# Kernel tuning notes

Measured on AMD Instinct MI355X. Metric: run time of the kernel, lower is better.

The kernel has to match this reference:

```python
import jax, jax.numpy as jnp
import numpy as np

B, N, HN, HE, H = 8, 128, 256, 128, 8
DH = HN // H
P = N * (N - 1) // 2


def _ln(x, g, b, eps=1e-5):
    m = jnp.mean(x, axis=-1, keepdims=True)
    v = jnp.mean((x - m) ** 2, axis=-1, keepdims=True)
    return (x - m) * jax.lax.rsqrt(v + eps) * g + b


def setup_inputs() -> dict:
    key = jax.random.key(0)
    ks = jax.random.split(key, 16)
    i1, i2 = np.triu_indices(N, k=1)  # all unordered pairs, P = N(N-1)/2
    s = lambda fan: 1.0 / np.sqrt(fan)
    return {
        "node_feat": jax.random.normal(ks[0], (B, N, HN), jnp.float32),
        "edge_feat": jax.random.normal(ks[1], (B, P, HE), jnp.float32),
        "x_idx1": jnp.asarray(i1, jnp.int32),
        "x_idx2": jnp.asarray(i2, jnp.int32),
        "mask_valid": jax.random.bernoulli(ks[2], 0.9, (B, P)).astype(jnp.float32),
        "Wqkv": jax.random.normal(ks[3], (HN, 3 * HN), jnp.float32) * s(HN),
        "bqkv": jnp.zeros((3 * HN,), jnp.float32),
        "Wev": jax.random.normal(ks[4], (HE, HN), jnp.float32) * s(HE),
        "bev": jnp.zeros((HN,), jnp.float32),
        "Wea": jax.random.normal(ks[5], (HE, H), jnp.float32) * s(HE),
        "bea": jnp.zeros((H,), jnp.float32),
        "Wo": jax.random.normal(ks[6], (2 * HN, HN), jnp.float32) * s(2 * HN),
        "bo": jnp.zeros((HN,), jnp.float32),
        "Wsk": jax.random.normal(ks[7], (HN, 2 * HN), jnp.float32) * s(HN),
        "bsk": jnp.zeros((2 * HN,), jnp.float32),
        "gn": jnp.ones((HN,), jnp.float32),
        "bn": jnp.zeros((HN,), jnp.float32),
        "ge": jnp.ones((HE,), jnp.float32),
        "be": jnp.zeros((HE,), jnp.float32),
    }


def reference(node_feat, edge_feat, x_idx1, x_idx2, mask_valid,
              Wqkv, bqkv, Wev, bev, Wea, bea, Wo, bo, Wsk, bsk,
              gn, bn, ge, be):
    n_in = _ln(node_feat, gn, bn)                      # [B,N,HN]
    e_in = _ln(edge_feat, ge, be)                      # [B,P,HE]
    q, k, v = jnp.split(n_in @ Wqkv + bqkv, 3, axis=-1)
    to_h = lambda t: t.reshape(B, -1, H, DH).transpose(0, 2, 1, 3)
    q, k, v = to_h(q), to_h(k), to_h(v)                # [B,H,N,DH]
    e_val = to_h(e_in @ Wev + bev)                     # [B,H,P,DH]
    e_adj = (e_in @ Wea + bea).transpose(0, 2, 1)      # [B,H,P]

    scale = DH ** -0.5
    logits = jnp.einsum('bhqd,bhkd->bhqk', q, k) * scale  # [B,H,N,N]
    # per-pair logits; torch stacks [qk, edge_adj] then sums -> just add
    l_node1 = logits[:, :, x_idx1, x_idx2] + e_adj     # node i1 attends to i2
    l_node2 = logits[:, :, x_idx2, x_idx1] + e_adj     # node i2 attends to i1
    v_node1 = e_val + v[:, :, x_idx2]                  # value node i1 receives
    v_node2 = e_val + v[:, :, x_idx1]

    # group the 2P directed edges by destination node (= torch cat+sort+reshape)
    cat_idx = jnp.concatenate([x_idx1, x_idx2])        # [2P]
    order = jnp.argsort(cat_idx)                       # stable sort
    gl = jnp.concatenate([l_node1, l_node2], axis=2)[:, :, order].reshape(B, H, N, N - 1)
    gv = jnp.concatenate([v_node1, v_node2], axis=2)[:, :, order].reshape(B, H, N, N - 1, DH)
    gm = jnp.concatenate([mask_valid, mask_valid], axis=1)[:, order].reshape(B, N, N - 1)[:, None]  # [B,1,N,N-1]

    gl = jnp.where(gm == 0.0, -9e15, gl)
    probs = jax.nn.softmax(gl, axis=3)
    probs = probs * jnp.any(gm != 0.0, axis=3, keepdims=True).astype(probs.dtype)
    attn = jnp.einsum('bhnk,bhnkd->bhnd', probs, gv)   # [B,H,N,DH]
    attn = attn.transpose(0, 2, 1, 3).reshape(B, N, HN)

    comb = jax.nn.gelu(jnp.concatenate([n_in, attn], axis=-1) @ Wo + bo, approximate=False)
    val, gate = jnp.split(comb @ Wsk + bsk, 2, axis=-1)
    g = jax.nn.sigmoid(gate)
    return node_feat * (1.0 - g) + val * g
```

## Files before the change

### kernel.cpp

```cpp
#include <hip/hip_runtime.h>
#include <hip/hip_bf16.h>
#include <math.h>

#define BB 8
#define NN 128
#define HN 256
#define HE 128
#define NH 8
#define DH 32
#define PP 8128
#define BP (BB*PP)

typedef __hip_bfloat16 bf16;
typedef __hip_bfloat162 bf162;
typedef __attribute__((ext_vector_type(8))) short bf16x8;
typedef __attribute__((ext_vector_type(4))) float f32x4;

__device__ __forceinline__ float bf2f(bf16 x){ return __bfloat162float(x); }
__device__ __forceinline__ float bfraw2f(short u){
  return __uint_as_float(((unsigned)(unsigned short)u) << 16);
}

__device__ __forceinline__ float wave_sum(float v){
  #pragma unroll
  for (int off=32; off>=1; off>>=1) v += __shfl_xor(v, off, 64);
  return v;
}
__device__ __forceinline__ float wave_max(float v){
  #pragma unroll
  for (int off=32; off>=1; off>>=1) v = fmaxf(v, __shfl_xor(v, off, 64));
  return v;
}
__device__ __forceinline__ float g16_sum(float v){
  #pragma unroll
  for (int off=8; off>=1; off>>=1) v += __shfl_xor(v, off, 16);
  return v;
}

__device__ __forceinline__ int pair_idx(int a, int c){
  int i = a < c ? a : c;
  int j = a < c ? c : a;
  return ((i*(255 - i))>>1) + (j - i - 1);
}

#define C_NODE 0LL
#define C_MASK 262144LL
#define C_WQKV 327168LL
#define C_BQKV 523776LL
#define C_WEV  524544LL
#define C_BEV  557312LL
#define C_WEA  557568LL
#define C_BEA  558592LL
#define C_WO   558600LL
#define C_BO   689672LL
#define C_WSK  689928LL
#define C_BSK  821000LL
#define C_GN   821512LL
#define C_BN   821768LL
#define C_GE   822024LL
#define C_BE   822152LL
#define IOFF   822400LL
#define TOT8   102785
#define I_NIN  0LL
#define I_Q    262144LL
#define I_K    524288LL
#define I_V    786432LL
#define I_ATTN 1048576LL
#define I_COMB 1310720LL
#define I_EA2  1572864LL
#define I_XG   2093056LL
#define I_EVAL 6254592LL
#define I_WT   14577664LL
#define I_FLG  14594048LL

struct SrcPtrs { const void* p[16]; };

__global__ __launch_bounds__(256) void k_convert(SrcPtrs sp, float* __restrict__ dst,
                                                 int* __restrict__ flags,
                                                 const unsigned short* __restrict__ nodeRaw)
{
  __shared__ int sbad;
  if (threadIdx.x == 0) sbad = 0;
  __syncthreads();
  {
    int bad = 0;
    for (int i = threadIdx.x; i < 1024; i += 256){
      unsigned e = (nodeRaw[i] >> 7) & 0xFFu;
      if (e >= 194u) bad = 1;
    }
    if (bad) sbad = 1;
  }
  __syncthreads();
  const int f32 = sbad;
  if (blockIdx.x == 0 && threadIdx.x == 0) flags[0] = f32;
  int o = blockIdx.x*256 + threadIdx.x;
  if (o >= TOT8) return;
  const int cum[17] = {0,32768,40896,65472,65568,69664,69696,69824,69825,
                       86209,86241,102625,102689,102721,102753,102769,102785};
  int s = 0;
  #pragma unroll
  for (int i = 1; i <= 15; i++) if (o >= cum[i]) s = i;
  const int li = o - cum[s];
  float4 r0, r1;
  if (f32){
    const float4* src = (const float4*)sp.p[s];
    r0 = src[2*li]; r1 = src[2*li+1];
  } else {
    union { float4 f; unsigned short u[8]; } cv;
    cv.f = ((const float4*)sp.p[s])[li];
    r0.x = __uint_as_float((unsigned)cv.u[0] << 16);
    r0.y = __uint_as_float((unsigned)cv.u[1] << 16);
    r0.z = __uint_as_float((unsigned)cv.u[2] << 16);
    r0.w = __uint_as_float((unsigned)cv.u[3] << 16);
    r1.x = __uint_as_float((unsigned)cv.u[4] << 16);
    r1.y = __uint_as_float((unsigned)cv.u[5] << 16);
    r1.z = __uint_as_float((unsigned)cv.u[6] << 16);
    r1.w = __uint_as_float((unsigned)cv.u[7] << 16);
  }
  float4* d = (float4*)(dst + (long long)cum[s]*8);
  d[2*li]   = r0;
  d[2*li+1] = r1;
}

__global__ __launch_bounds__(256) void k2w_transpose(const float* __restrict__ cWev,
                                                     bf16* __restrict__ Wt)
{
  int idx = blockIdx.x*256 + threadIdx.x;
  int k = idx >> 8, n = idx & 255;
  Wt[n*128 + k] = __float2bfloat16(cWev[idx]);
}

__global__ __launch_bounds__(256) void k1_node_ln_qkv(
    const float* __restrict__ cnode, const float* __restrict__ cWqkv,
    const float* __restrict__ cbqkv, const float* __restrict__ cgn, const float* __restrict__ cbn,
    float* __restrict__ nin_ws, float* __restrict__ q_ws, float* __restrict__ k_ws,
    float* __restrict__ v_ws)
{
  __shared__ float xln[4][HN];
  const int t = threadIdx.x, wv = t>>6, lane = t&63;
  const int g0 = blockIdx.x*4;
  {
    int g = g0 + wv;
    float x[4];
    #pragma unroll
    for (int i=0;i<4;i++) x[i] = cnode[g*HN + lane + 64*i];
    float s = x[0]+x[1]+x[2]+x[3];
    s = wave_sum(s);
    float m = s * (1.0f/HN);
    float q = 0.f;
    #pragma unroll
    for (int i=0;i<4;i++){ float d = x[i]-m; q += d*d; }
    q = wave_sum(q);
    float rstd = rsqrtf(fmaxf(q*(1.0f/HN), 0.f) + 1e-5f);
    #pragma unroll
    for (int i=0;i<4;i++){
      int c = lane + 64*i;
      float y = (x[i]-m)*rstd*cgn[c] + cbn[c];
      xln[wv][c] = y;
      nin_ws[g*HN + c] = y;
    }
  }
  __syncthreads();
  float acc[4][3];
  #pragma unroll
  for (int c=0;c<3;c++){
    float bb = cbqkv[t + 256*c];
    #pragma unroll
    for (int r=0;r<4;r++) acc[r][c] = bb;
  }
  for (int k=0;k<HN;k+=4){
    float4 xv[4];
    #pragma unroll
    for (int r=0;r<4;r++) xv[r] = *reinterpret_cast<const float4*>(&xln[r][k]);
    #pragma unroll
    for (int kk=0;kk<4;kk++){
      float w0 = cWqkv[(k+kk)*768 + t];
      float w1 = cWqkv[(k+kk)*768 + t + 256];
      float w2 = cWqkv[(k+kk)*768 + t + 512];
      #pragma unroll
      for (int r=0;r<4;r++){
        float xr = (&xv[r].x)[kk];
        acc[r][0] = fmaf(xr, w0, acc[r][0]);
        acc[r][1] = fmaf(xr, w1, acc[r][1]);
        acc[r][2] = fmaf(xr, w2, acc[r][2]);
      }
    }
  }
  const int h = t>>5, d = t&31;
  #pragma unroll
  for (int r=0;r<4;r++){
    int g = g0 + r;
    int b = g>>7, n = g&127;
    int o = ((b*NH + h)*NN + n)*DH + d;
    q_ws[o] = acc[r][0]; k_ws[o] = acc[r][1]; v_ws[o] = acc[r][2];
  }
}

__global__ __launch_bounds__(256) void k2a_edge_ln(
    const void* __restrict__ edge_raw, const float* __restrict__ cWea,
    const float* __restrict__ cbea, const float* __restrict__ cge,
    const float* __restrict__ cbe, const float* __restrict__ cmask,
    bf16* __restrict__ xg, float* __restrict__ ea2, const int* __restrict__ flags)
{
  __shared__ float xlnS[16][136];
  const int t = threadIdx.x;
  const int R0 = blockIdx.x*16;
  const int b = R0 / PP;
  const int p0 = R0 - b*PP;
  const int f32 = flags[0];
  {
    int r = t>>4, sub = t&15;
    long base = (long)(R0 + r)*HE + sub*8;
    float x[8];
    if (f32){
      const float* cef = (const float*)edge_raw + base;
      float4 a0 = *reinterpret_cast<const float4*>(cef);
      float4 a1 = *reinterpret_cast<const float4*>(cef + 4);
      x[0]=a0.x; x[1]=a0.y; x[2]=a0.z; x[3]=a0.w;
      x[4]=a1.x; x[5]=a1.y; x[6]=a1.z; x[7]=a1.w;
    } else {
      union { float4 f; short u[8]; } cv;
      cv.f = *reinterpret_cast<const float4*>((const bf16*)edge_raw + base);
      #pragma unroll
      for (int i=0;i<8;i++) x[i] = bfraw2f(cv.u[i]);
    }
    float s = 0.f;
    #pragma unroll
    for (int i=0;i<8;i++) s += x[i];
    s = g16_sum(s);
    float m = s*(1.0f/HE);
    float q = 0.f;
    #pragma unroll
    for (int i=0;i<8;i++){ float dd = x[i]-m; q += dd*dd; }
    q = g16_sum(q);
    float rstd = rsqrtf(fmaxf(q*(1.0f/HE), 0.f) + 1e-5f);
    #pragma unroll
    for (int i=0;i<8;i++){
      int c = sub*8 + i;
      xlnS[r][c] = (x[i]-m)*rstd*cge[c] + cbe[c];
    }
  }
  __syncthreads();
  {
    int r = t>>4, c0 = (t&15)*8;
    union { float4 f; bf16 h[8]; } o;
    #pragma unroll
    for (int i=0;i<8;i++) o.h[i] = __float2bfloat16(xlnS[r][c0+i]);
    *reinterpret_cast<float4*>(xg + (long)(R0 + r)*HE + c0) = o.f;
  }
  if (t < 128){
    int r = t>>3, c = t&7;
    float s = cbea[c];
    for (int k=0;k<HE;k++) s = fmaf(xlnS[r][k], cWea[k*NH + c], s);
    int p = p0 + r;
    float mk = cmask[b*PP + p];
    ea2[(b*NH + c)*PP + p] = (mk != 0.0f) ? s : -9e15f;
  }
}

__global__ __launch_bounds__(256) void k2b_mfma(
    const bf16* __restrict__ xg, const bf16* __restrict__ Wt,
    const float* __restrict__ cbev, bf16* __restrict__ e_val)
{
  __shared__ bf16 Xs[64][136];
  __shared__ bf16 Ws[64][136];
  const int t = threadIdx.x;
  const int rowblk = blockIdx.x >> 2;
  const int cb = blockIdx.x & 3;
  const int b = rowblk / 127;
  const int p0 = (rowblk - b*127) * 64;
  const int n0 = cb * 64;
  #pragma unroll
  for (int it = 0; it < 4; ++it){
    int idx = it*256 + t;
    int r = idx >> 4, seg = idx & 15;
    float4 xv = *reinterpret_cast<const float4*>(xg + (long)(b*PP + p0 + r)*HE + seg*8);
    *reinterpret_cast<float4*>(&Xs[r][seg*8]) = xv;
    float4 wv = *reinterpret_cast<const float4*>(Wt + (long)(n0 + r)*HE + seg*8);
    *reinterpret_cast<float4*>(&Ws[r][seg*8]) = wv;
  }
  __syncthreads();
  const int wv = t>>6, lane = t&63;
  const int fm = lane & 15, q = lane >> 4;
  f32x4 acc[4];
  #pragma unroll
  for (int ct=0; ct<4; ++ct){
    float bb = cbev[n0 + ct*16 + fm];
    acc[ct][0]=bb; acc[ct][1]=bb; acc[ct][2]=bb; acc[ct][3]=bb;
  }
  #pragma unroll
  for (int ks=0; ks<4; ++ks){
    bf16x8 A = *reinterpret_cast<const bf16x8*>(&Xs[wv*16 + fm][ks*32 + q*8]);
    #pragma unroll
    for (int ct=0; ct<4; ++ct){
      bf16x8 Bf = *reinterpret_cast<const bf16x8*>(&Ws[ct*16 + fm][ks*32 + q*8]);
      acc[ct] = __builtin_amdgcn_mfma_f32_16x16x32_bf16(A, Bf, acc[ct], 0, 0, 0);
    }
  }
  #pragma unroll
  for (int ct=0; ct<4; ++ct){
    int col = n0 + ct*16 + fm;
    int h = col >> 5, d = col & 31;
    #pragma unroll
    for (int reg=0; reg<4; ++reg){
      int p = p0 + wv*16 + q*4 + reg;
      e_val[((long)(b*NH + h)*PP + p)*DH + d] = __float2bfloat16(acc[ct][reg]);
    }
  }
}

__global__ __launch_bounds__(256) void k3_attn(
    const float* __restrict__ q_ws, const float* __restrict__ k_ws, const float* __restrict__ v_ws,
    const bf16* __restrict__ e_val, const float* __restrict__ ea2,
    float* __restrict__ attn)
{
  __shared__ float kT[DH][NN+1];
  __shared__ float vS[NN][DH+1];
  __shared__ float qS[8][DH];
  __shared__ float pbuf[4][NN];
  const int t = threadIdx.x, wv = t>>6, lane = t&63;
  const int s16 = blockIdx.x & 15, h = (blockIdx.x>>4)&7, b = blockIdx.x>>7;
  const int bh = b*NH + h;
  const int n0 = s16*8;
  const float* kb = k_ws + (long)bh*NN*DH;
  const float* vb = v_ws + (long)bh*NN*DH;
  const float* qb = q_ws + ((long)bh*NN + n0)*DH;
  for (int idx=t; idx<NN*DH; idx+=256){
    int m = idx>>5, d = idx&31;
    kT[d][m] = kb[idx];
    vS[m][d] = vb[idx];
  }
  if (t < 8*DH) reinterpret_cast<float*>(qS)[t] = qb[t];
  __syncthreads();
  const float scale = 0.17677669529663687f;
  const float* eab = ea2 + (long)bh*PP;
  const bf16* evp = e_val + (long)bh*PP*DH;
  for (int it=0; it<2; ++it){
    const int nn = it*4 + wv;
    const int n = n0 + nn;
    const int m1 = lane, m2 = lane + 64;
    float dot1 = 0.f, dot2 = 0.f;
    #pragma unroll
    for (int d=0; d<DH; d++){
      float qd = qS[nn][d];
      dot1 = fmaf(qd, kT[d][m1], dot1);
      dot2 = fmaf(qd, kT[d][m2], dot2);
    }
    const bool self1 = (m1 == n), self2 = (m2 == n);
    int pr1 = pair_idx(n, self1 ? (m1^1) : m1);
    int pr2 = pair_idx(n, self2 ? (m2^1) : m2);
    float ea1 = eab[pr1], ea2v = eab[pr2];
    float l1 = self1 ? -INFINITY : dot1*scale + ea1;
    float l2 = self2 ? -INFINITY : dot2*scale + ea2v;
    bool av = (!self1 && ea1 > -8.9e15f) || (!self2 && ea2v > -8.9e15f);
    float lm = wave_max(fmaxf(l1, l2));
    float e1 = __expf(l1 - lm), e2 = __expf(l2 - lm);
    float ssum = wave_sum(e1 + e2);
    int anyv = __any((int)av);
    float inv = anyv ? (1.0f/ssum) : 0.0f;
    pbuf[wv][m1] = e1*inv;
    pbuf[wv][m2] = e2*inv;
    const int msub = lane & 15, oct = lane >> 4;
    float acc[8];
    #pragma unroll
    for (int e=0;e<8;e++) acc[e] = 0.f;
    #pragma unroll
    for (int mm=0; mm<128; mm+=16){
      int m = mm + msub;
      int ms = (m==n) ? (m^1) : m;
      int pr = pair_idx(n, ms);
      bf16x8 ev8 = *reinterpret_cast<const bf16x8*>(evp + (long)pr*DH + oct*8);
      float pm = pbuf[wv][m];
      const float* vrow = &vS[m][oct*8];
      #pragma unroll
      for (int e=0;e<8;e++){
        acc[e] = fmaf(pm, vrow[e] + bfraw2f(ev8[e]), acc[e]);
      }
    }
    #pragma unroll
    for (int off=1; off<16; off<<=1){
      #pragma unroll
      for (int e=0;e<8;e++) acc[e] += __shfl_xor(acc[e], off, 64);
    }
    if (msub == 0){
      float* op = attn + ((long)b*NN + n)*HN + h*DH + oct*8;
      float4 o0 = {acc[0],acc[1],acc[2],acc[3]};
      float4 o1 = {acc[4],acc[5],acc[6],acc[7]};
      *reinterpret_cast<float4*>(op) = o0;
      *reinterpret_cast<float4*>(op+4) = o1;
    }
  }
}

__global__ __launch_bounds__(256) void k4_wo_gelu(
    const float* __restrict__ nin_ws, const float* __restrict__ attn,
    const float* __restrict__ cWo, const float* __restrict__ cbo,
    float* __restrict__ comb)
{
  __shared__ float xc[4][2*HN];
  const int t = threadIdx.x, wv = t>>6, lane = t&63;
  const int g0 = blockIdx.x*4;
  {
    int g = g0 + wv;
    #pragma unroll
    for (int i=0;i<4;i++){
      int c = lane + 64*i;
      xc[wv][c] = nin_ws[g*HN + c];
      xc[wv][HN + c] = attn[g*HN + c];
    }
  }
  __syncthreads();
  float acc[4];
  float bb = cbo[t];
  #pragma unroll
  for (int r=0;r<4;r++) acc[r] = bb;
  for (int k=0;k<2*HN;k+=4){
    float4 xv[4];
    #pragma unroll
    for (int r=0;r<4;r++) xv[r] = *reinterpret_cast<const float4*>(&xc[r][k]);
    #pragma unroll
    for (int kk=0;kk<4;kk++){
      float w = cWo[(k+kk)*HN + t];
      #pragma unroll
      for (int r=0;r<4;r++) acc[r] = fmaf((&xv[r].x)[kk], w, acc[r]);
    }
  }
  #pragma unroll
  for (int r=0;r<4;r++){
    float x = acc[r];
    float y = 0.5f*x*(1.0f + erff(x*0.7071067811865475f));
    comb[(g0+r)*HN + t] = y;
  }
}

__global__ __launch_bounds__(256) void k5_sk_gate(
    const float* __restrict__ comb, const float* __restrict__ cnode,
    const float* __restrict__ cWsk, const float* __restrict__ cbsk,
    void* __restrict__ out, const int* __restrict__ flags)
{
  __shared__ float xc[4][HN];
  const int t = threadIdx.x, wv = t>>6, lane = t&63;
  const int g0 = blockIdx.x*4;
  #pragma unroll
  for (int i=0;i<4;i++){
    int c = lane + 64*i;
    xc[wv][c] = comb[(g0+wv)*HN + c];
  }
  __syncthreads();
  const int f32 = flags[0];
  float accv[4], accg[4];
  float bv = cbsk[t], bg = cbsk[t+256];
  #pragma unroll
  for (int r=0;r<4;r++){ accv[r]=bv; accg[r]=bg; }
  for (int k=0;k<HN;k+=4){
    float4 xv[4];
    #pragma unroll
    for (int r=0;r<4;r++) xv[r] = *reinterpret_cast<const float4*>(&xc[r][k]);
    #pragma unroll
    for (int kk=0;kk<4;kk++){
      float w0 = cWsk[(k+kk)*512 + t];
      float w1 = cWsk[(k+kk)*512 + t + 256];
      #pragma unroll
      for (int r=0;r<4;r++){
        float xr = (&xv[r].x)[kk];
        accv[r] = fmaf(xr, w0, accv[r]);
        accg[r] = fmaf(xr, w1, accg[r]);
      }
    }
  }
  #pragma unroll
  for (int r=0;r<4;r++){
    int g = g0 + r;
    float gg = 1.0f/(1.0f + __expf(-accg[r]));
    float nf = cnode[g*HN + t];
    float res = nf*(1.0f - gg) + accv[r]*gg;
    if (f32) ((float*)out)[g*HN + t] = res;
    else ((bf16*)out)[g*HN + t] = __float2bfloat16(res);
  }
}

extern "C" void kernel_launch(void* const* d_in, const int* in_sizes, int n_inputs,
                              void* d_out, int out_size, void* d_ws, size_t ws_size,
                              hipStream_t stream)
{
  float* ws = (float*)d_ws;
  float* c_node = ws + C_NODE;
  float* c_mask = ws + C_MASK;
  float* c_Wqkv = ws + C_WQKV;
  float* c_bqkv = ws + C_BQKV;
  float* c_Wev  = ws + C_WEV;
  float* c_bev  = ws + C_BEV;
  float* c_Wea  = ws + C_WEA;
  float* c_bea  = ws + C_BEA;
  float* c_Wo   = ws + C_WO;
  float* c_bo   = ws + C_BO;
  float* c_Wsk  = ws + C_WSK;
  float* c_bsk  = ws + C_BSK;
  float* c_gn   = ws + C_GN;
  float* c_bn   = ws + C_BN;
  float* c_ge   = ws + C_GE;
  float* c_be   = ws + C_BE;
  float* base   = ws + IOFF;
  float* nin_ws  = base + I_NIN;
  float* q_ws    = base + I_Q;
  float* k_ws    = base + I_K;
  float* v_ws    = base + I_V;
  float* attn_ws = base + I_ATTN;
  float* comb_ws = base + I_COMB;
  float* ea2_ws  = base + I_EA2;
  bf16*  xg_ws   = (bf16*)(base + I_XG);
  bf16*  eval_ws = (bf16*)(base + I_EVAL);
  bf16*  wt_ws   = (bf16*)(base + I_WT);
  int*   flags   = (int*)(base + I_FLG);

  SrcPtrs sp;
  sp.p[0]  = d_in[0];
  sp.p[1]  = d_in[4];
  sp.p[2]  = d_in[5];
  sp.p[3]  = d_in[6];
  sp.p[4]  = d_in[7];
  sp.p[5]  = d_in[8];
  sp.p[6]  = d_in[9];
  sp.p[7]  = d_in[10];
  sp.p[8]  = d_in[11];
  sp.p[9]  = d_in[12];
  sp.p[10] = d_in[13];
  sp.p[11] = d_in[14];
  sp.p[12] = d_in[15];
  sp.p[13] = d_in[16];
  sp.p[14] = d_in[17];
  sp.p[15] = d_in[18];

  k_convert<<<(TOT8 + 255)/256, 256, 0, stream>>>(sp, ws, flags,
                                                  (const unsigned short*)d_in[0]);
  k2w_transpose<<<128, 256, 0, stream>>>(c_Wev, wt_ws);
  k1_node_ln_qkv<<<256, 256, 0, stream>>>(c_node, c_Wqkv, c_bqkv, c_gn, c_bn,
                                          nin_ws, q_ws, k_ws, v_ws);
  k2a_edge_ln<<<BP/16, 256, 0, stream>>>(d_in[1], c_Wea, c_bea, c_ge, c_be, c_mask,
                                         xg_ws, ea2_ws, flags);
  k2b_mfma<<<1016*4, 256, 0, stream>>>(xg_ws, wt_ws, c_bev, eval_ws);
  k3_attn<<<BB*NH*16, 256, 0, stream>>>(q_ws, k_ws, v_ws, eval_ws, ea2_ws, attn_ws);
  k4_wo_gelu<<<256, 256, 0, stream>>>(nin_ws, attn_ws, c_Wo, c_bo, comb_ws);
  k5_sk_gate<<<256, 256, 0, stream>>>(comb_ws, c_node, c_Wsk, c_bsk, d_out, flags);
}
```

Measured before the change: 233.3 us.

## Fuse Wev transpose into convert, merge Wo/Wsk kernels, restructure edge MFMA

```diff
diff --git a/kernel.cpp b/kernel.cpp
--- a/kernel.cpp
+++ b/kernel.cpp
@@ -61,23 +61,25 @@
 #define C_BE   822152LL
 #define IOFF   822400LL
 #define TOT8   102785
+#define CONVBLKS 402
 #define I_NIN  0LL
 #define I_Q    262144LL
 #define I_K    524288LL
 #define I_V    786432LL
 #define I_ATTN 1048576LL
-#define I_COMB 1310720LL
-#define I_EA2  1572864LL
-#define I_XG   2093056LL
-#define I_EVAL 6254592LL
-#define I_WT   14577664LL
-#define I_FLG  14594048LL
+#define I_EA2  1310720LL
+#define I_XG   1830912LL
+#define I_EVAL 5992448LL
+#define I_WT   14315520LL
+#define I_FLG  14331904LL
 
 struct SrcPtrs { const void* p[16]; };
 
 __global__ __launch_bounds__(256) void k_convert(SrcPtrs sp, float* __restrict__ dst,
                                                  int* __restrict__ flags,
-                                                 const unsigned short* __restrict__ nodeRaw)
+                                                 const unsigned short* __restrict__ nodeRaw,
+                                                 const void* __restrict__ rawWev,
+                                                 bf16* __restrict__ Wt)
 {
   __shared__ int sbad;
   if (threadIdx.x == 0) sbad = 0;
@@ -93,6 +95,15 @@
   __syncthreads();
   const int f32 = sbad;
   if (blockIdx.x == 0 && threadIdx.x == 0) flags[0] = f32;
+
+  if (blockIdx.x >= CONVBLKS){
+    int idx = (blockIdx.x - CONVBLKS)*256 + threadIdx.x;
+    float v = f32 ? ((const float*)rawWev)[idx]
+                  : bfraw2f(((const short*)rawWev)[idx]);
+    Wt[(idx & 255)*128 + (idx >> 8)] = __float2bfloat16(v);
+    return;
+  }
+
   int o = blockIdx.x*256 + threadIdx.x;
   if (o >= TOT8) return;
   const int cum[17] = {0,32768,40896,65472,65568,69664,69696,69824,69825,
@@ -122,14 +133,6 @@
   d[2*li+1] = r1;
 }
 
-__global__ __launch_bounds__(256) void k2w_transpose(const float* __restrict__ cWev,
-                                                     bf16* __restrict__ Wt)
-{
-  int idx = blockIdx.x*256 + threadIdx.x;
-  int k = idx >> 8, n = idx & 255;
-  Wt[n*128 + k] = __float2bfloat16(cWev[idx]);
-}
-
 __global__ __launch_bounds__(256) void k1_node_ln_qkv(
     const float* __restrict__ cnode, const float* __restrict__ cWqkv,
     const float* __restrict__ cbqkv, const float* __restrict__ cgn, const float* __restrict__ cbn,
@@ -203,6 +206,7 @@
     bf16* __restrict__ xg, float* __restrict__ ea2, const int* __restrict__ flags)
 {
   __shared__ float xlnS[16][136];
+  __shared__ float part[128];
   const int t = threadIdx.x;
   const int R0 = blockIdx.x*16;
   const int b = R0 / PP;
@@ -248,13 +252,21 @@
     for (int i=0;i<8;i++) o.h[i] = __float2bfloat16(xlnS[r][c0+i]);
     *reinterpret_cast<float4*>(xg + (long)(R0 + r)*HE + c0) = o.f;
   }
-  if (t < 128){
-    int r = t>>3, c = t&7;
-    float s = cbea[c];
-    for (int k=0;k<HE;k++) s = fmaf(xlnS[r][k], cWea[k*NH + c], s);
-    int p = p0 + r;
-    float mk = cmask[b*PP + p];
-    ea2[(b*NH + c)*PP + p] = (mk != 0.0f) ? s : -9e15f;
+  {
+    const int c = t & 7, r = (t>>3) & 15, half = t>>7;
+    const int pid = r*8 + c;
+    float s = half ? 0.0f : cbea[c];
+    const int k0 = half*64;
+    #pragma unroll 8
+    for (int k=k0; k<k0+64; k++) s = fmaf(xlnS[r][k], cWea[k*NH + c], s);
+    if (half){ part[pid] = s; }
+    __syncthreads();
+    if (!half){
+      s += part[pid];
+      int p = p0 + r;
+      float mk = cmask[b*PP + p];
+      ea2[(b*NH + c)*PP + p] = (mk != 0.0f) ? s : -9e15f;
+    }
   }
 }
 
@@ -263,49 +275,39 @@
     const float* __restrict__ cbev, bf16* __restrict__ e_val)
 {
   __shared__ bf16 Xs[64][136];
-  __shared__ bf16 Ws[64][136];
   const int t = threadIdx.x;
-  const int rowblk = blockIdx.x >> 2;
-  const int cb = blockIdx.x & 3;
-  const int b = rowblk / 127;
-  const int p0 = (rowblk - b*127) * 64;
-  const int n0 = cb * 64;
+  const int b = blockIdx.x / 127;
+  const int rb = blockIdx.x - b*127;
+  const int p0 = rb * 64;
   #pragma unroll
   for (int it = 0; it < 4; ++it){
     int idx = it*256 + t;
     int r = idx >> 4, seg = idx & 15;
     float4 xv = *reinterpret_cast<const float4*>(xg + (long)(b*PP + p0 + r)*HE + seg*8);
     *reinterpret_cast<float4*>(&Xs[r][seg*8]) = xv;
-    float4 wv = *reinterpret_cast<const float4*>(Wt + (long)(n0 + r)*HE + seg*8);
-    *reinterpret_cast<float4*>(&Ws[r][seg*8]) = wv;
   }
   __syncthreads();
   const int wv = t>>6, lane = t&63;
   const int fm = lane & 15, q = lane >> 4;
-  f32x4 acc[4];
-  #pragma unroll
-  for (int ct=0; ct<4; ++ct){
-    float bb = cbev[n0 + ct*16 + fm];
-    acc[ct][0]=bb; acc[ct][1]=bb; acc[ct][2]=bb; acc[ct][3]=bb;
-  }
-  #pragma unroll
-  for (int ks=0; ks<4; ++ks){
-    bf16x8 A = *reinterpret_cast<const bf16x8*>(&Xs[wv*16 + fm][ks*32 + q*8]);
-    #pragma unroll
-    for (int ct=0; ct<4; ++ct){
-      bf16x8 Bf = *reinterpret_cast<const bf16x8*>(&Ws[ct*16 + fm][ks*32 + q*8]);
-      acc[ct] = __builtin_amdgcn_mfma_f32_16x16x32_bf16(A, Bf, acc[ct], 0, 0, 0);
-    }
-  }
-  #pragma unroll
-  for (int ct=0; ct<4; ++ct){
-    int col = n0 + ct*16 + fm;
-    int h = col >> 5, d = col & 31;
-    #pragma unroll
-    for (int reg=0; reg<4; ++reg){
-      int p = p0 + wv*16 + q*4 + reg;
-      e_val[((long)(b*NH + h)*PP + p)*DH + d] = __float2bfloat16(acc[ct][reg]);
-    }
+  bf16x8 A[4];
+  #pragma unroll
+  for (int ks=0; ks<4; ++ks)
+    A[ks] = *reinterpret_cast<const bf16x8*>(&Xs[wv*16 + fm][ks*32 + q*8]);
+  #pragma unroll
+  for (int ct=0; ct<16; ++ct){
+    const int col = ct*16 + fm;
+    float bb = cbev[col];
+    f32x4 acc = {bb, bb, bb, bb};
+    const bf16* wp = Wt + col*128 + q*8;
+    #pragma unroll
+    for (int ks=0; ks<4; ++ks){
+      bf16x8 Bf = *reinterpret_cast<const bf16x8*>(wp + ks*32);
+      acc = __builtin_amdgcn_mfma_f32_16x16x32_bf16(A[ks], Bf, acc, 0, 0, 0);
+    }
+    const int h = col >> 5, d = col & 31;
+    bf16* op = e_val + ((long)(b*NH + h)*PP + p0 + wv*16 + q*4)*DH + d;
+    #pragma unroll
+    for (int reg=0; reg<4; ++reg) op[reg*DH] = __float2bfloat16(acc[reg]);
   }
 }
 
@@ -392,12 +394,15 @@
   }
 }
 
-__global__ __launch_bounds__(256) void k4_wo_gelu(
+__global__ __launch_bounds__(256) void k45_out(
     const float* __restrict__ nin_ws, const float* __restrict__ attn,
     const float* __restrict__ cWo, const float* __restrict__ cbo,
-    float* __restrict__ comb)
+    const float* __restrict__ cWsk, const float* __restrict__ cbsk,
+    const float* __restrict__ cnode, void* __restrict__ out,
+    const int* __restrict__ flags)
 {
   __shared__ float xc[4][2*HN];
+  __shared__ float xc2[4][HN];
   const int t = threadIdx.x, wv = t>>6, lane = t&63;
   const int g0 = blockIdx.x*4;
   {
@@ -410,41 +415,27 @@
     }
   }
   __syncthreads();
-  float acc[4];
-  float bb = cbo[t];
-  #pragma unroll
-  for (int r=0;r<4;r++) acc[r] = bb;
-  for (int k=0;k<2*HN;k+=4){
-    float4 xv[4];
-    #pragma unroll
-    for (int r=0;r<4;r++) xv[r] = *reinterpret_cast<const float4*>(&xc[r][k]);
-    #pragma unroll
-    for (int kk=0;kk<4;kk++){
-      float w = cWo[(k+kk)*HN + t];
-      #pragma unroll
-      for (int r=0;r<4;r++) acc[r] = fmaf((&xv[r].x)[kk], w, acc[r]);
-    }
-  }
-  #pragma unroll
-  for (int r=0;r<4;r++){
-    float x = acc[r];
-    float y = 0.5f*x*(1.0f + erff(x*0.7071067811865475f));
-    comb[(g0+r)*HN + t] = y;
-  }
-}
-
-__global__ __launch_bounds__(256) void k5_sk_gate(
-    const float* __restrict__ comb, const float* __restrict__ cnode,
-    const float* __restrict__ cWsk, const float* __restrict__ cbsk,
-    void* __restrict__ out, const int* __restrict__ flags)
-{
-  __shared__ float xc[4][HN];
-  const int t = threadIdx.x, wv = t>>6, lane = t&63;
-  const int g0 = blockIdx.x*4;
-  #pragma unroll
-  for (int i=0;i<4;i++){
-    int c = lane + 64*i;
-    xc[wv][c] = comb[(g0+wv)*HN + c];
+  {
+    float acc[4];
+    float bb = cbo[t];
+    #pragma unroll
+    for (int r=0;r<4;r++) acc[r] = bb;
+    for (int k=0;k<2*HN;k+=4){
+      float4 xv[4];
+      #pragma unroll
+      for (int r=0;r<4;r++) xv[r] = *reinterpret_cast<const float4*>(&xc[r][k]);
+      #pragma unroll
+      for (int kk=0;kk<4;kk++){
+        float w = cWo[(k+kk)*HN + t];
+        #pragma unroll
+        for (int r=0;r<4;r++) acc[r] = fmaf((&xv[r].x)[kk], w, acc[r]);
+      }
+    }
+    #pragma unroll
+    for (int r=0;r<4;r++){
+      float x = acc[r];
+      xc2[r][t] = 0.5f*x*(1.0f + erff(x*0.7071067811865475f));
+    }
   }
   __syncthreads();
   const int f32 = flags[0];
@@ -455,7 +446,7 @@
   for (int k=0;k<HN;k+=4){
     float4 xv[4];
     #pragma unroll
-    for (int r=0;r<4;r++) xv[r] = *reinterpret_cast<const float4*>(&xc[r][k]);
+    for (int r=0;r<4;r++) xv[r] = *reinterpret_cast<const float4*>(&xc2[r][k]);
     #pragma unroll
     for (int kk=0;kk<4;kk++){
       float w0 = cWsk[(k+kk)*512 + t];
@@ -488,7 +479,6 @@
   float* c_mask = ws + C_MASK;
   float* c_Wqkv = ws + C_WQKV;
   float* c_bqkv = ws + C_BQKV;
-  float* c_Wev  = ws + C_WEV;
   float* c_bev  = ws + C_BEV;
   float* c_Wea  = ws + C_WEA;
   float* c_bea  = ws + C_BEA;
@@ -506,7 +496,6 @@
   float* k_ws    = base + I_K;
   float* v_ws    = base + I_V;
   float* attn_ws = base + I_ATTN;
-  float* comb_ws = base + I_COMB;
   float* ea2_ws  = base + I_EA2;
   bf16*  xg_ws   = (bf16*)(base + I_XG);
   bf16*  eval_ws = (bf16*)(base + I_EVAL);
@@ -531,15 +520,15 @@
   sp.p[14] = d_in[17];
   sp.p[15] = d_in[18];
 
-  k_convert<<<(TOT8 + 255)/256, 256, 0, stream>>>(sp, ws, flags,
-                                                  (const unsigned short*)d_in[0]);
-  k2w_transpose<<<128, 256, 0, stream>>>(c_Wev, wt_ws);
+  k_convert<<<CONVBLKS + 128, 256, 0, stream>>>(sp, ws, flags,
+                                                (const unsigned short*)d_in[0],
+                                                d_in[7], wt_ws);
   k1_node_ln_qkv<<<256, 256, 0, stream>>>(c_node, c_Wqkv, c_bqkv, c_gn, c_bn,
                                           nin_ws, q_ws, k_ws, v_ws);
   k2a_edge_ln<<<BP/16, 256, 0, stream>>>(d_in[1], c_Wea, c_bea, c_ge, c_be, c_mask,
                                          xg_ws, ea2_ws, flags);
-  k2b_mfma<<<1016*4, 256, 0, stream>>>(xg_ws, wt_ws, c_bev, eval_ws);
+  k2b_mfma<<<1016, 256, 0, stream>>>(xg_ws, wt_ws, c_bev, eval_ws);
   k3_attn<<<BB*NH*16, 256, 0, stream>>>(q_ws, k_ws, v_ws, eval_ws, ea2_ws, attn_ws);
-  k4_wo_gelu<<<256, 256, 0, stream>>>(nin_ws, attn_ws, c_Wo, c_bo, comb_ws);
-  k5_sk_gate<<<256, 256, 0, stream>>>(comb_ws, c_node, c_Wsk, c_bsk, d_out, flags);
-}
+  k45_out<<<256, 256, 0, stream>>>(nin_ws, attn_ws, c_Wo, c_bo, c_Wsk, c_bsk,
+                                   c_node, d_out, flags);
+}
```

Result: slower. 249.3 us (+6.9%).
